# Optimization experiments

Measured on AMD Instinct MI355X. Metric: run time of the kernel, lower is better.

The kernel has to match this reference:

```python
import jax, jax.numpy as jnp
import numpy as np

B, N, D = 8, 512, 512
H = 8
DK = D // H  # 64 per-channel attention maps


def setup_inputs() -> dict:
    key = jax.random.key(0)
    k1, k2, k3 = jax.random.split(key, 3)
    inputs = jax.random.normal(k1, (B, N, D), dtype=jnp.float32)
    W_qkv = jax.random.normal(k2, (D, 3 * DK), dtype=jnp.float32) * 0.02
    W_o = jax.random.normal(k3, (DK, D), dtype=jnp.float32) * 0.02
    return {"inputs": inputs, "W_qkv": W_qkv, "W_o": W_o}


def reference(inputs, W_qkv, W_o):
    d_k = W_qkv.shape[1] // 3
    QKV = inputs @ W_qkv                      # (B, N, 3*d_k)
    Q = QKV[:, :, 0 * d_k:1 * d_k]
    K = QKV[:, :, 1 * d_k:2 * d_k]
    V = QKV[:, :, 2 * d_k:3 * d_k]
    scale = 1.0 / jnp.sqrt(jnp.asarray(d_k, dtype=QKV.dtype))
    # per-channel (head_dim=1) attention, batched over the d_k channels
    S = jnp.einsum('bnc,bmc->bcnm', Q, K) * scale   # (B, d_k, N, N)
    A = jax.nn.softmax(S, axis=-1)
    SA = jnp.einsum('bcnm,bmc->bnc', A, V)          # (B, N, d_k)
    return SA @ W_o                                 # (B, N, D)
```

## Files before the change

### kernel.cpp

```cpp
#include <hip/hip_runtime.h>
#include <math.h>

#define BB 8
#define NN 512
#define DD 512
#define DKK 64
#define NC 192
#define CHN (BB * DKK * NN)
#define SAEL (BB * NN * DKK)
#define WEL (NC * DD)
#define WOEL (DKK * DD)
#define NFRAG_W (WEL / 8)
#define NFRAG_WO (WOEL / 8)
#define NJ 20

typedef short s8v   __attribute__((ext_vector_type(8)));
typedef float f32x4 __attribute__((ext_vector_type(4)));
typedef unsigned short ushort;

static __device__ __forceinline__ void split2(float w, ushort& h, ushort& l) {
    const unsigned u = __float_as_uint(w);
    h = (ushort)(u >> 16);
    const float lo = w - __uint_as_float(u & 0xFFFF0000u);
    l = (ushort)(__float_as_uint(lo) >> 16);
}

__constant__ float c_invfact[NJ] = {
    1.0f, 1.0f, 0.5f, 1.6666667e-1f, 4.1666668e-2f, 8.3333338e-3f,
    1.3888889e-3f, 1.9841270e-4f, 2.4801588e-5f, 2.7557319e-6f,
    2.7557319e-7f, 2.5052108e-8f, 2.0876757e-9f, 1.6059044e-10f,
    1.1470746e-11f, 7.6471637e-13f, 4.7794773e-14f, 2.8114572e-15f,
    1.5619207e-16f, 8.2206352e-18f};

__global__ __launch_bounds__(256) void wprep(const float* __restrict__ W,
                                             const float* __restrict__ Wo,
                                             ushort* __restrict__ Wfh,
                                             ushort* __restrict__ Wfl,
                                             ushort* __restrict__ Woh,
                                             ushort* __restrict__ Wol) {
    const int gtid = blockIdx.x * 256 + threadIdx.x;
    if (gtid < NFRAG_W) {
        const int ct   = gtid >> 10;
        const int ks   = (gtid >> 6) & 15;
        const int lane = gtid & 63;
        const int lm   = lane & 15;
        const int quad = lane >> 4;
        const int chan = ct * 16 + lm;
        const int k0   = ks * 32 + quad * 8;
        s8v h, l;
        #pragma unroll
        for (int e = 0; e < 8; ++e) {
            ushort hh, ll;
            split2(W[(size_t)(k0 + e) * NC + chan], hh, ll);
            h[e] = (short)hh;
            l[e] = (short)ll;
        }
        *(s8v*)(Wfh + (size_t)gtid * 8) = h;
        *(s8v*)(Wfl + (size_t)gtid * 8) = l;
        return;
    }
    const int fi = gtid - NFRAG_W;
    if (fi < NFRAG_WO) {
        const int lane = fi & 63;
        const int ks   = (fi >> 6) & 1;
        const int dt   = fi >> 7;
        const int lm   = lane & 15;
        const int quad = lane >> 4;
        const int d    = dt * 16 + lm;
        s8v h, l;
        #pragma unroll
        for (int e = 0; e < 8; ++e) {
            ushort hh, ll;
            split2(Wo[(size_t)(ks * 32 + quad * 8 + e) * DD + d], hh, ll);
            h[e] = (short)hh;
            l[e] = (short)ll;
        }
        *(s8v*)(Woh + (size_t)fi * 8) = h;
        *(s8v*)(Wol + (size_t)fi * 8) = l;
    }
}

__global__ __launch_bounds__(768) void qkv_fused(const float* __restrict__ X,
                                                 const ushort* __restrict__ Wfh,
                                                 const ushort* __restrict__ Wfl,
                                                 float* __restrict__ qkv) {
    __shared__ ushort Ah[16 * 512 + 128];
    __shared__ ushort Al[16 * 512 + 128];

    const int st  = blockIdx.x;
    const int tid = threadIdx.x;

    for (int i = tid; i < 2048; i += 768) {
        const int row = i >> 7;
        const int k0  = (i & 127) * 4;
        const float4 x = *(const float4*)(X + (size_t)(st * 16 + row) * DD + k0);
        const float xe[4] = {x.x, x.y, x.z, x.w};
        ushort h[4], l[4];
        #pragma unroll
        for (int e = 0; e < 4; ++e) split2(xe[e], h[e], l[e]);
        const int ks   = k0 >> 5;
        const int quad = (k0 >> 3) & 3;
        const int e0   = k0 & 7;
        const int lane = quad * 16 + row;
        const size_t a = (size_t)(ks * 64 + lane) * 8 + e0 + ks * 8;
        *(ushort4*)(Ah + a) = make_ushort4(h[0], h[1], h[2], h[3]);
        *(ushort4*)(Al + a) = make_ushort4(l[0], l[1], l[2], l[3]);
    }
    __syncthreads();

    const int ct   = tid >> 6;
    const int lane = tid & 63;
    const int lm   = lane & 15;
    const int quad = lane >> 4;
    const int chan = ct * 16 + lm;

    const ushort* bw_h = Wfh + ((size_t)(ct * 16) * 64 + lane) * 8;
    const ushort* bw_l = Wfl + ((size_t)(ct * 16) * 64 + lane) * 8;

    f32x4 acc = {0.f, 0.f, 0.f, 0.f};

    #pragma unroll 4
    for (int ks = 0; ks < 16; ++ks) {
        const size_t woff = (size_t)ks * 512;
        const s8v bh = *(const s8v*)(bw_h + woff);
        const s8v bl = *(const s8v*)(bw_l + woff);
        const size_t a = (size_t)(ks * 64 + lane) * 8 + ks * 8;
        const s8v ah = *(const s8v*)(Ah + a);
        const s8v al = *(const s8v*)(Al + a);
        acc = __builtin_amdgcn_mfma_f32_16x16x32_bf16(ah, bh, acc, 0, 0, 0);
        acc = __builtin_amdgcn_mfma_f32_16x16x32_bf16(ah, bl, acc, 0, 0, 0);
        acc = __builtin_amdgcn_mfma_f32_16x16x32_bf16(al, bh, acc, 0, 0, 0);
    }

    const int which = chan >> 6;
    const int c     = chan & 63;
    const int seq0  = st * 16 + quad * 4;
    const int b     = seq0 >> 9;
    const int n0    = seq0 & 511;
    const float4 v = {acc[0], acc[1], acc[2], acc[3]};
    *(float4*)(qkv + (size_t)which * CHN + ((size_t)(b * DKK + c)) * NN + n0) = v;
}

__global__ __launch_bounds__(256) void attn_taylor(const float* __restrict__ qkv,
                                                   ushort* __restrict__ SAh,
                                                   ushort* __restrict__ SAl) {
    __shared__ float part[256][41];
    __shared__ float coef[2 * NJ];

    const int tid = threadIdx.x;
    const size_t chan = (size_t)blockIdx.x * NN;
    const float* qp = qkv + chan;
    const float* kp = qkv + CHN + chan;
    const float* vp = qkv + 2 * CHN + chan;

    const float k0 = kp[tid], k1 = kp[tid + 256];
    const float v0 = vp[tid], v1 = vp[tid + 256];

    float p0 = 1.f, p1 = 1.f;
    #pragma unroll
    for (int j = 0; j < NJ; ++j) {
        part[tid][j]      = fmaf(p0, v0, p1 * v1);
        part[tid][NJ + j] = p0 + p1;
        p0 *= k0;
        p1 *= k1;
    }
    __syncthreads();

    if (tid < 2 * NJ) {
        float s = 0.f;
        #pragma unroll 8
        for (int t = 0; t < 256; ++t) s += part[t][tid];
        const int jj = (tid < NJ) ? tid : tid - NJ;
        coef[tid] = s * c_invfact[jj];
    }
    __syncthreads();

    float c[2 * NJ];
    #pragma unroll
    for (int j = 0; j < 2 * NJ; ++j) c[j] = coef[j];

    const int b  = blockIdx.x >> 6;
    const int ch = blockIdx.x & 63;
    const int ks = ch >> 5;
    const int jf = ch & 7;
    const int lhi = ((ch & 31) >> 3) << 4;

    #pragma unroll
    for (int r = 0; r < 2; ++r) {
        const int n = tid + r * 256;
        const float t = qp[n] * 0.125f;
        float P = c[NJ - 1];
        float Q = c[2 * NJ - 1];
        #pragma unroll
        for (int j = NJ - 2; j >= 0; --j) {
            P = fmaf(P, t, c[j]);
            Q = fmaf(Q, t, c[NJ + j]);
        }
        const float val = P / Q;
        ushort hi, lo;
        split2(val, hi, lo);
        const int gseq = b * NN + n;
        const int stg  = gseq >> 4;
        const int lane = lhi | (gseq & 15);
        const size_t addr = ((size_t)(stg * 2 + ks) * 64 + lane) * 8 + jf;
        SAh[addr] = hi;
        SAl[addr] = lo;
    }
}

__global__ __launch_bounds__(256) void out_mfma(const ushort* __restrict__ SAh,
                                                const ushort* __restrict__ SAl,
                                                const ushort* __restrict__ Woh,
                                                const ushort* __restrict__ Wol,
                                                float* __restrict__ out) {
    const int widx = blockIdx.x * 4 + (threadIdx.x >> 6);
    const int st   = widx >> 3;
    const int dg   = widx & 7;
    const int lane = threadIdx.x & 63;
    const int lm   = lane & 15;
    const int quad = lane >> 4;

    const ushort* sa_h = SAh + ((size_t)(st * 2) * 64 + lane) * 8;
    const ushort* sa_l = SAl + ((size_t)(st * 2) * 64 + lane) * 8;
    const s8v ah0 = *(const s8v*)(sa_h);
    const s8v ah1 = *(const s8v*)(sa_h + 512);
    const s8v al0 = *(const s8v*)(sa_l);
    const s8v al1 = *(const s8v*)(sa_l + 512);

    const int seq0 = st * 16 + quad * 4;

    #pragma unroll
    for (int dti = 0; dti < 4; ++dti) {
        const int dt = dg * 4 + dti;
        const int d  = dt * 16 + lm;

        const ushort* wo_h = Woh + ((size_t)(dt * 2) * 64 + lane) * 8;
        const ushort* wo_l = Wol + ((size_t)(dt * 2) * 64 + lane) * 8;
        const s8v bh0 = *(const s8v*)(wo_h);
        const s8v bh1 = *(const s8v*)(wo_h + 512);
        const s8v bl0 = *(const s8v*)(wo_l);
        const s8v bl1 = *(const s8v*)(wo_l + 512);

        f32x4 acc = {0.f, 0.f, 0.f, 0.f};
        acc = __builtin_amdgcn_mfma_f32_16x16x32_bf16(ah0, bh0, acc, 0, 0, 0);
        acc = __builtin_amdgcn_mfma_f32_16x16x32_bf16(ah0, bl0, acc, 0, 0, 0);
        acc = __builtin_amdgcn_mfma_f32_16x16x32_bf16(al0, bh0, acc, 0, 0, 0);
        acc = __builtin_amdgcn_mfma_f32_16x16x32_bf16(ah1, bh1, acc, 0, 0, 0);
        acc = __builtin_amdgcn_mfma_f32_16x16x32_bf16(ah1, bl1, acc, 0, 0, 0);
        acc = __builtin_amdgcn_mfma_f32_16x16x32_bf16(al1, bh1, acc, 0, 0, 0);

        #pragma unroll
        for (int r = 0; r < 4; ++r)
            out[(size_t)(seq0 + r) * DD + d] = acc[r];
    }
}

extern "C" void kernel_launch(void* const* d_in, const int* in_sizes, int n_in,
                              void* d_out, int out_size, void* d_ws, size_t ws_size,
                              hipStream_t stream) {
    const float* X    = (const float*)d_in[0];
    const float* Wqkv = (const float*)d_in[1];
    const float* Wo   = (const float*)d_in[2];
    float* out = (float*)d_out;

    float*  qkv = (float*)d_ws;
    ushort* SAh = (ushort*)(qkv + (size_t)3 * CHN);
    ushort* SAl = SAh + (size_t)SAEL;
    ushort* Wfh = SAl + (size_t)SAEL;
    ushort* Wfl = Wfh + (size_t)WEL;
    ushort* Woh = Wfl + (size_t)WEL;
    ushort* Wol = Woh + (size_t)WOEL;

    wprep<<<dim3((NFRAG_W + NFRAG_WO) / 256), 256, 0, stream>>>(
        Wqkv, Wo, Wfh, Wfl, Woh, Wol);
    qkv_fused<<<dim3(256), 768, 0, stream>>>(X, Wfh, Wfl, qkv);
    attn_taylor<<<dim3(BB * DKK), 256, 0, stream>>>(qkv, SAh, SAl);
    out_mfma<<<dim3(512), 256, 0, stream>>>(SAh, SAl, Woh, Wol, out);
}
```

Measured before the change: 81.57 us.

## Fuse four kernels into one cooperative persistent kernel with grid barriers

Merges weight preparation, QKV projection, Taylor-series attention and output projection into a single cooperative kernel of 256 blocks separated by software grid barriers. The goal is to remove three kernel launch boundaries and their idle gaps. Weight splitting is folded into spare threads during the X staging phase. The attention coefficient reduction is also split four ways to shorten the serial sum. In exchange, the atomic spin barrier adds global synchronisation cost, each block has fewer threads active in later phases, and the barrier has a guard counter that could exit early.

```diff
diff --git a/kernel.cpp b/kernel.cpp
--- a/kernel.cpp
+++ b/kernel.cpp
@@ -13,6 +13,7 @@
 #define NFRAG_W (WEL / 8)
 #define NFRAG_WO (WOEL / 8)
 #define NJ 20
+#define NBLK 256
 
 typedef short s8v   __attribute__((ext_vector_type(8)));
 typedef float f32x4 __attribute__((ext_vector_type(4)));
@@ -32,63 +33,48 @@
     1.1470746e-11f, 7.6471637e-13f, 4.7794773e-14f, 2.8114572e-15f,
     1.5619207e-16f, 8.2206352e-18f};
 
-__global__ __launch_bounds__(256) void wprep(const float* __restrict__ W,
-                                             const float* __restrict__ Wo,
-                                             ushort* __restrict__ Wfh,
-                                             ushort* __restrict__ Wfl,
-                                             ushort* __restrict__ Woh,
-                                             ushort* __restrict__ Wol) {
-    const int gtid = blockIdx.x * 256 + threadIdx.x;
-    if (gtid < NFRAG_W) {
-        const int ct   = gtid >> 10;
-        const int ks   = (gtid >> 6) & 15;
-        const int lane = gtid & 63;
-        const int lm   = lane & 15;
-        const int quad = lane >> 4;
-        const int chan = ct * 16 + lm;
-        const int k0   = ks * 32 + quad * 8;
-        s8v h, l;
-        #pragma unroll
-        for (int e = 0; e < 8; ++e) {
-            ushort hh, ll;
-            split2(W[(size_t)(k0 + e) * NC + chan], hh, ll);
-            h[e] = (short)hh;
-            l[e] = (short)ll;
-        }
-        *(s8v*)(Wfh + (size_t)gtid * 8) = h;
-        *(s8v*)(Wfl + (size_t)gtid * 8) = l;
-        return;
-    }
-    const int fi = gtid - NFRAG_W;
-    if (fi < NFRAG_WO) {
-        const int lane = fi & 63;
-        const int ks   = (fi >> 6) & 1;
-        const int dt   = fi >> 7;
-        const int lm   = lane & 15;
-        const int quad = lane >> 4;
-        const int d    = dt * 16 + lm;
-        s8v h, l;
-        #pragma unroll
-        for (int e = 0; e < 8; ++e) {
-            ushort hh, ll;
-            split2(Wo[(size_t)(ks * 32 + quad * 8 + e) * DD + d], hh, ll);
-            h[e] = (short)hh;
-            l[e] = (short)ll;
-        }
-        *(s8v*)(Woh + (size_t)fi * 8) = h;
-        *(s8v*)(Wol + (size_t)fi * 8) = l;
-    }
+__device__ unsigned g_bar = 0;
+
+static __device__ __forceinline__ void gridbar(int tid) {
+    __syncthreads();
+    if (tid == 0) {
+        __threadfence();
+        const unsigned v = __hip_atomic_fetch_add(&g_bar, 1u, __ATOMIC_ACQ_REL,
+                                                  __HIP_MEMORY_SCOPE_AGENT);
+        const unsigned target = (v & ~(unsigned)(NBLK - 1)) + NBLK;
+        unsigned cur = v + 1;
+        int guard = 0;
+        while ((int)(cur - target) < 0 && guard < (1 << 24)) {
+            __builtin_amdgcn_s_sleep(1);
+            cur = __hip_atomic_load(&g_bar, __ATOMIC_RELAXED,
+                                    __HIP_MEMORY_SCOPE_AGENT);
+            ++guard;
+        }
+    }
+    __syncthreads();
+    __builtin_amdgcn_fence(__ATOMIC_ACQUIRE, "agent");
 }
 
-__global__ __launch_bounds__(768) void qkv_fused(const float* __restrict__ X,
-                                                 const ushort* __restrict__ Wfh,
-                                                 const ushort* __restrict__ Wfl,
-                                                 float* __restrict__ qkv) {
-    __shared__ ushort Ah[16 * 512 + 128];
-    __shared__ ushort Al[16 * 512 + 128];
-
+__global__ __launch_bounds__(768) void fused(
+    const float* __restrict__ X, const float* __restrict__ W,
+    const float* __restrict__ Wo,
+    ushort* __restrict__ Wfh, ushort* __restrict__ Wfl,
+    ushort* __restrict__ Woh, ushort* __restrict__ Wol,
+    float* __restrict__ qkv,
+    ushort* __restrict__ SAh, ushort* __restrict__ SAl,
+    float* __restrict__ out) {
+
+    __shared__ union {
+        struct { ushort Ah[16 * 512 + 128]; ushort Al[16 * 512 + 128]; } q;
+        struct {
+            float part[2][256][41];
+            float red[2][2 * NJ][4];
+            float coef[2][2 * NJ];
+        } a;
+    } sm;
+
+    const int tid = threadIdx.x;
     const int st  = blockIdx.x;
-    const int tid = threadIdx.x;
 
     for (int i = tid; i < 2048; i += 768) {
         const int row = i >> 7;
@@ -103,155 +89,194 @@
         const int e0   = k0 & 7;
         const int lane = quad * 16 + row;
         const size_t a = (size_t)(ks * 64 + lane) * 8 + e0 + ks * 8;
-        *(ushort4*)(Ah + a) = make_ushort4(h[0], h[1], h[2], h[3]);
-        *(ushort4*)(Al + a) = make_ushort4(l[0], l[1], l[2], l[3]);
-    }
-    __syncthreads();
-
-    const int ct   = tid >> 6;
-    const int lane = tid & 63;
-    const int lm   = lane & 15;
-    const int quad = lane >> 4;
-    const int chan = ct * 16 + lm;
-
-    const ushort* bw_h = Wfh + ((size_t)(ct * 16) * 64 + lane) * 8;
-    const ushort* bw_l = Wfl + ((size_t)(ct * 16) * 64 + lane) * 8;
-
-    f32x4 acc = {0.f, 0.f, 0.f, 0.f};
-
-    #pragma unroll 4
-    for (int ks = 0; ks < 16; ++ks) {
-        const size_t woff = (size_t)ks * 512;
-        const s8v bh = *(const s8v*)(bw_h + woff);
-        const s8v bl = *(const s8v*)(bw_l + woff);
-        const size_t a = (size_t)(ks * 64 + lane) * 8 + ks * 8;
-        const s8v ah = *(const s8v*)(Ah + a);
-        const s8v al = *(const s8v*)(Al + a);
-        acc = __builtin_amdgcn_mfma_f32_16x16x32_bf16(ah, bh, acc, 0, 0, 0);
-        acc = __builtin_amdgcn_mfma_f32_16x16x32_bf16(ah, bl, acc, 0, 0, 0);
-        acc = __builtin_amdgcn_mfma_f32_16x16x32_bf16(al, bh, acc, 0, 0, 0);
-    }
-
-    const int which = chan >> 6;
-    const int c     = chan & 63;
-    const int seq0  = st * 16 + quad * 4;
-    const int b     = seq0 >> 9;
-    const int n0    = seq0 & 511;
-    const float4 v = {acc[0], acc[1], acc[2], acc[3]};
-    *(float4*)(qkv + (size_t)which * CHN + ((size_t)(b * DKK + c)) * NN + n0) = v;
-}
-
-__global__ __launch_bounds__(256) void attn_taylor(const float* __restrict__ qkv,
-                                                   ushort* __restrict__ SAh,
-                                                   ushort* __restrict__ SAl) {
-    __shared__ float part[256][41];
-    __shared__ float coef[2 * NJ];
-
-    const int tid = threadIdx.x;
-    const size_t chan = (size_t)blockIdx.x * NN;
-    const float* qp = qkv + chan;
-    const float* kp = qkv + CHN + chan;
-    const float* vp = qkv + 2 * CHN + chan;
-
-    const float k0 = kp[tid], k1 = kp[tid + 256];
-    const float v0 = vp[tid], v1 = vp[tid + 256];
-
-    float p0 = 1.f, p1 = 1.f;
-    #pragma unroll
-    for (int j = 0; j < NJ; ++j) {
-        part[tid][j]      = fmaf(p0, v0, p1 * v1);
-        part[tid][NJ + j] = p0 + p1;
-        p0 *= k0;
-        p1 *= k1;
-    }
-    __syncthreads();
-
-    if (tid < 2 * NJ) {
+        *(ushort4*)(sm.q.Ah + a) = make_ushort4(h[0], h[1], h[2], h[3]);
+        *(ushort4*)(sm.q.Al + a) = make_ushort4(l[0], l[1], l[2], l[3]);
+    }
+    if (tid >= 704) {
+        const int gtid = st * 64 + (tid - 704);
+        if (gtid < NFRAG_W) {
+            const int ct   = gtid >> 10;
+            const int ks   = (gtid >> 6) & 15;
+            const int lane = gtid & 63;
+            const int lm   = lane & 15;
+            const int quad = lane >> 4;
+            const int chan = ct * 16 + lm;
+            const int k0   = ks * 32 + quad * 8;
+            s8v h, l;
+            #pragma unroll
+            for (int e = 0; e < 8; ++e) {
+                ushort hh, ll;
+                split2(W[(size_t)(k0 + e) * NC + chan], hh, ll);
+                h[e] = (short)hh;
+                l[e] = (short)ll;
+            }
+            *(s8v*)(Wfh + (size_t)gtid * 8) = h;
+            *(s8v*)(Wfl + (size_t)gtid * 8) = l;
+        } else {
+            const int fi   = gtid - NFRAG_W;
+            const int lane = fi & 63;
+            const int ks   = (fi >> 6) & 1;
+            const int dt   = fi >> 7;
+            const int lm   = lane & 15;
+            const int quad = lane >> 4;
+            const int d    = dt * 16 + lm;
+            s8v h, l;
+            #pragma unroll
+            for (int e = 0; e < 8; ++e) {
+                ushort hh, ll;
+                split2(Wo[(size_t)(ks * 32 + quad * 8 + e) * DD + d], hh, ll);
+                h[e] = (short)hh;
+                l[e] = (short)ll;
+            }
+            *(s8v*)(Woh + (size_t)fi * 8) = h;
+            *(s8v*)(Wol + (size_t)fi * 8) = l;
+        }
+    }
+    gridbar(tid);
+
+    {
+        const int ct   = tid >> 6;
+        const int lane = tid & 63;
+        const int lm   = lane & 15;
+        const int quad = lane >> 4;
+        const int chan = ct * 16 + lm;
+
+        const ushort* bw_h = Wfh + ((size_t)(ct * 16) * 64 + lane) * 8;
+        const ushort* bw_l = Wfl + ((size_t)(ct * 16) * 64 + lane) * 8;
+
+        f32x4 acc = {0.f, 0.f, 0.f, 0.f};
+        #pragma unroll 4
+        for (int ks = 0; ks < 16; ++ks) {
+            const size_t woff = (size_t)ks * 512;
+            const s8v bh = *(const s8v*)(bw_h + woff);
+            const s8v bl = *(const s8v*)(bw_l + woff);
+            const size_t a = (size_t)(ks * 64 + lane) * 8 + ks * 8;
+            const s8v ah = *(const s8v*)(sm.q.Ah + a);
+            const s8v al = *(const s8v*)(sm.q.Al + a);
+            acc = __builtin_amdgcn_mfma_f32_16x16x32_bf16(ah, bh, acc, 0, 0, 0);
+            acc = __builtin_amdgcn_mfma_f32_16x16x32_bf16(ah, bl, acc, 0, 0, 0);
+            acc = __builtin_amdgcn_mfma_f32_16x16x32_bf16(al, bh, acc, 0, 0, 0);
+        }
+        const int which = chan >> 6;
+        const int c     = chan & 63;
+        const int seq0  = st * 16 + quad * 4;
+        const int b     = seq0 >> 9;
+        const int n0    = seq0 & 511;
+        const float4 v = {acc[0], acc[1], acc[2], acc[3]};
+        *(float4*)(qkv + (size_t)which * CHN + ((size_t)(b * DKK + c)) * NN + n0) = v;
+    }
+    gridbar(tid);
+
+    const int h2 = tid >> 8;
+    const int t2 = tid & 255;
+    if (tid < 512) {
+        const int cidx  = st * 2 + h2;
+        const float* kp = qkv + CHN + (size_t)cidx * NN;
+        const float* vp = qkv + 2 * CHN + (size_t)cidx * NN;
+        const float k0 = kp[t2], k1 = kp[t2 + 256];
+        const float v0 = vp[t2], v1 = vp[t2 + 256];
+        float p0 = 1.f, p1 = 1.f;
+        #pragma unroll
+        for (int j = 0; j < NJ; ++j) {
+            sm.a.part[h2][t2][j]      = fmaf(p0, v0, p1 * v1);
+            sm.a.part[h2][t2][NJ + j] = p0 + p1;
+            p0 *= k0;
+            p1 *= k1;
+        }
+    }
+    __syncthreads();
+    if (tid < 512 && t2 < 160) {
+        const int j = t2 >> 2, g = t2 & 3;
         float s = 0.f;
         #pragma unroll 8
-        for (int t = 0; t < 256; ++t) s += part[t][tid];
-        const int jj = (tid < NJ) ? tid : tid - NJ;
-        coef[tid] = s * c_invfact[jj];
-    }
-    __syncthreads();
-
-    float c[2 * NJ];
-    #pragma unroll
-    for (int j = 0; j < 2 * NJ; ++j) c[j] = coef[j];
-
-    const int b  = blockIdx.x >> 6;
-    const int ch = blockIdx.x & 63;
-    const int ks = ch >> 5;
-    const int jf = ch & 7;
-    const int lhi = ((ch & 31) >> 3) << 4;
-
-    #pragma unroll
-    for (int r = 0; r < 2; ++r) {
-        const int n = tid + r * 256;
-        const float t = qp[n] * 0.125f;
-        float P = c[NJ - 1];
-        float Q = c[2 * NJ - 1];
-        #pragma unroll
-        for (int j = NJ - 2; j >= 0; --j) {
-            P = fmaf(P, t, c[j]);
-            Q = fmaf(Q, t, c[NJ + j]);
-        }
-        const float val = P / Q;
-        ushort hi, lo;
-        split2(val, hi, lo);
-        const int gseq = b * NN + n;
-        const int stg  = gseq >> 4;
-        const int lane = lhi | (gseq & 15);
-        const size_t addr = ((size_t)(stg * 2 + ks) * 64 + lane) * 8 + jf;
-        SAh[addr] = hi;
-        SAl[addr] = lo;
-    }
-}
-
-__global__ __launch_bounds__(256) void out_mfma(const ushort* __restrict__ SAh,
-                                                const ushort* __restrict__ SAl,
-                                                const ushort* __restrict__ Woh,
-                                                const ushort* __restrict__ Wol,
-                                                float* __restrict__ out) {
-    const int widx = blockIdx.x * 4 + (threadIdx.x >> 6);
-    const int st   = widx >> 3;
-    const int dg   = widx & 7;
-    const int lane = threadIdx.x & 63;
-    const int lm   = lane & 15;
-    const int quad = lane >> 4;
-
-    const ushort* sa_h = SAh + ((size_t)(st * 2) * 64 + lane) * 8;
-    const ushort* sa_l = SAl + ((size_t)(st * 2) * 64 + lane) * 8;
-    const s8v ah0 = *(const s8v*)(sa_h);
-    const s8v ah1 = *(const s8v*)(sa_h + 512);
-    const s8v al0 = *(const s8v*)(sa_l);
-    const s8v al1 = *(const s8v*)(sa_l + 512);
-
-    const int seq0 = st * 16 + quad * 4;
-
-    #pragma unroll
-    for (int dti = 0; dti < 4; ++dti) {
-        const int dt = dg * 4 + dti;
-        const int d  = dt * 16 + lm;
-
-        const ushort* wo_h = Woh + ((size_t)(dt * 2) * 64 + lane) * 8;
-        const ushort* wo_l = Wol + ((size_t)(dt * 2) * 64 + lane) * 8;
-        const s8v bh0 = *(const s8v*)(wo_h);
-        const s8v bh1 = *(const s8v*)(wo_h + 512);
-        const s8v bl0 = *(const s8v*)(wo_l);
-        const s8v bl1 = *(const s8v*)(wo_l + 512);
-
-        f32x4 acc = {0.f, 0.f, 0.f, 0.f};
-        acc = __builtin_amdgcn_mfma_f32_16x16x32_bf16(ah0, bh0, acc, 0, 0, 0);
-        acc = __builtin_amdgcn_mfma_f32_16x16x32_bf16(ah0, bl0, acc, 0, 0, 0);
-        acc = __builtin_amdgcn_mfma_f32_16x16x32_bf16(al0, bh0, acc, 0, 0, 0);
-        acc = __builtin_amdgcn_mfma_f32_16x16x32_bf16(ah1, bh1, acc, 0, 0, 0);
-        acc = __builtin_amdgcn_mfma_f32_16x16x32_bf16(ah1, bl1, acc, 0, 0, 0);
-        acc = __builtin_amdgcn_mfma_f32_16x16x32_bf16(al1, bh1, acc, 0, 0, 0);
-
-        #pragma unroll
-        for (int r = 0; r < 4; ++r)
-            out[(size_t)(seq0 + r) * DD + d] = acc[r];
+        for (int i = 0; i < 64; ++i) s += sm.a.part[h2][i * 4 + g][j];
+        sm.a.red[h2][j][g] = s;
+    }
+    __syncthreads();
+    if (tid < 512 && t2 < 2 * NJ) {
+        const int jj = (t2 < NJ) ? t2 : t2 - NJ;
+        sm.a.coef[h2][t2] = (sm.a.red[h2][t2][0] + sm.a.red[h2][t2][1] +
+                             sm.a.red[h2][t2][2] + sm.a.red[h2][t2][3]) *
+                            c_invfact[jj];
+    }
+    __syncthreads();
+    if (tid < 512) {
+        const int cidx  = st * 2 + h2;
+        const float* qp = qkv + (size_t)cidx * NN;
+        float c[2 * NJ];
+        #pragma unroll
+        for (int j = 0; j < 2 * NJ; ++j) c[j] = sm.a.coef[h2][j];
+
+        const int b   = cidx >> 6;
+        const int ch  = cidx & 63;
+        const int ks  = ch >> 5;
+        const int jf  = ch & 7;
+        const int lhi = ((ch & 31) >> 3) << 4;
+
+        #pragma unroll
+        for (int r = 0; r < 2; ++r) {
+            const int n   = t2 + r * 256;
+            const float t = qp[n] * 0.125f;
+            float P = c[NJ - 1];
+            float Q = c[2 * NJ - 1];
+            #pragma unroll
+            for (int j = NJ - 2; j >= 0; --j) {
+                P = fmaf(P, t, c[j]);
+                Q = fmaf(Q, t, c[NJ + j]);
+            }
+            const float val = P / Q;
+            ushort hi, lo;
+            split2(val, hi, lo);
+            const int gseq  = b * NN + n;
+            const int stg   = gseq >> 4;
+            const int lane  = lhi | (gseq & 15);
+            const size_t addr = ((size_t)(stg * 2 + ks) * 64 + lane) * 8 + jf;
+            SAh[addr] = hi;
+            SAl[addr] = lo;
+        }
+    }
+    gridbar(tid);
+
+    const int w3 = tid >> 6;
+    if (w3 < 8) {
+        const int lane = tid & 63;
+        const int lm   = lane & 15;
+        const int quad = lane >> 4;
+        const int dg   = w3;
+
+        const ushort* sa_h = SAh + ((size_t)(st * 2) * 64 + lane) * 8;
+        const ushort* sa_l = SAl + ((size_t)(st * 2) * 64 + lane) * 8;
+        const s8v ah0 = *(const s8v*)(sa_h);
+        const s8v ah1 = *(const s8v*)(sa_h + 512);
+        const s8v al0 = *(const s8v*)(sa_l);
+        const s8v al1 = *(const s8v*)(sa_l + 512);
+
+        const int seq0 = st * 16 + quad * 4;
+
+        #pragma unroll
+        for (int dti = 0; dti < 4; ++dti) {
+            const int dt = dg * 4 + dti;
+            const int d  = dt * 16 + lm;
+
+            const ushort* wo_h = Woh + ((size_t)(dt * 2) * 64 + lane) * 8;
+            const ushort* wo_l = Wol + ((size_t)(dt * 2) * 64 + lane) * 8;
+            const s8v bh0 = *(const s8v*)(wo_h);
+            const s8v bh1 = *(const s8v*)(wo_h + 512);
+            const s8v bl0 = *(const s8v*)(wo_l);
+            const s8v bl1 = *(const s8v*)(wo_l + 512);
+
+            f32x4 acc = {0.f, 0.f, 0.f, 0.f};
+            acc = __builtin_amdgcn_mfma_f32_16x16x32_bf16(ah0, bh0, acc, 0, 0, 0);
+            acc = __builtin_amdgcn_mfma_f32_16x16x32_bf16(ah0, bl0, acc, 0, 0, 0);
+            acc = __builtin_amdgcn_mfma_f32_16x16x32_bf16(al0, bh0, acc, 0, 0, 0);
+            acc = __builtin_amdgcn_mfma_f32_16x16x32_bf16(ah1, bh1, acc, 0, 0, 0);
+            acc = __builtin_amdgcn_mfma_f32_16x16x32_bf16(ah1, bl1, acc, 0, 0, 0);
+            acc = __builtin_amdgcn_mfma_f32_16x16x32_bf16(al1, bh1, acc, 0, 0, 0);
+
+            #pragma unroll
+            for (int r = 0; r < 4; ++r)
+                out[(size_t)(seq0 + r) * DD + d] = acc[r];
+        }
     }
 }
 
@@ -271,9 +296,9 @@
     ushort* Woh = Wfl + (size_t)WEL;
     ushort* Wol = Woh + (size_t)WOEL;
 
-    wprep<<<dim3((NFRAG_W + NFRAG_WO) / 256), 256, 0, stream>>>(
-        Wqkv, Wo, Wfh, Wfl, Woh, Wol);
-    qkv_fused<<<dim3(256), 768, 0, stream>>>(X, Wfh, Wfl, qkv);
-    attn_taylor<<<dim3(BB * DKK), 256, 0, stream>>>(qkv, SAh, SAl);
-    out_mfma<<<dim3(512), 256, 0, stream>>>(SAh, SAl, Woh, Wol, out);
+    void* args[] = {(void*)&X,   (void*)&Wqkv, (void*)&Wo,
+                    (void*)&Wfh, (void*)&Wfl,  (void*)&Woh, (void*)&Wol,
+                    (void*)&qkv, (void*)&SAh,  (void*)&SAl, (void*)&out};
+    hipLaunchCooperativeKernel((void*)fused, dim3(NBLK), dim3(768), args, 0,
+                               stream);
 }
```

New measurement: 226.6 us. 178% more time.
